# Kernel tuning notes

Measured on AMD Instinct MI355X. Metric: run time of the kernel, lower is better.

## Reference

```python
import jax, jax.numpy as jnp
import numpy as np

N, F, OUT = 8192, 256, 256


def setup_inputs() -> dict:
    key = jax.random.key(0)
    ks = jax.random.split(key, 8)
    s = 1.0 / np.sqrt(F)
    return {
        "features": jax.random.normal(ks[0], (N, F), jnp.float32),
        "key_features": jax.random.normal(ks[1], (N, F), jnp.float32),
        "adj_matrix": jax.random.uniform(ks[2], (N, N), jnp.float32),
        "W_d": jax.random.normal(ks[3], (2 * F, F), jnp.float32) * (1.0 / np.sqrt(2 * F)),
        "b_d": jnp.zeros((F,), jnp.float32),
        "W_o": jax.random.normal(ks[4], (F, OUT), jnp.float32) * s,
        "b_o": jnp.zeros((OUT,), jnp.float32),
        "W_a": jax.random.normal(ks[5], (F, F), jnp.float32) * s,
        "b_a": jnp.zeros((F,), jnp.float32),
        "W_ao": jax.random.normal(ks[6], (F, OUT), jnp.float32) * s,
        "b_ao": jnp.zeros((OUT,), jnp.float32),
    }


def reference(features, key_features, adj_matrix, W_d, b_d, W_o, b_o, W_a, b_a, W_ao, b_ao):
    n = features.shape[0]
    # masked softmax over rows; self-loop (diagonal) masked out
    neg = jnp.asarray(-1e9, adj_matrix.dtype)
    logits = adj_matrix * 5.0 + jnp.eye(n, dtype=adj_matrix.dtype) * neg
    a = jax.nn.softmax(logits, axis=-1)  # [N, N]
    # sum_j a_ij * concat(x_i, x_j) == concat(x_i * rowsum_i, (A @ X)_i)
    rowsum = jnp.sum(a, axis=-1, keepdims=True)  # == 1, kept for faithfulness
    agg = a @ features  # [N, F]
    neigh = jnp.concatenate([features * rowsum, agg], axis=-1)  # [N, 2F]
    neigh_distill = neigh @ W_d + b_d
    feature_updated = jnp.tanh((features - neigh_distill) @ W_o + b_o)
    # aggregate branch (withAgg=True)
    key_agg = (a @ key_features) @ W_a + b_a
    feature_aggregate = jnp.tanh((key_features + key_agg) @ W_ao + b_ao)
    return (feature_updated, feature_aggregate)
```

## Files before the change

### kernel.cpp

```cpp
#include <hip/hip_runtime.h>
#include <stdint.h>
#include <math.h>


typedef __attribute__((ext_vector_type(8)))  short bf16x8_t;
typedef __attribute__((ext_vector_type(4)))  float f32x4_t;
typedef __attribute__((ext_vector_type(16))) float f32x16_t;

#define MFMA32(A, B, C) __builtin_amdgcn_mfma_f32_32x32x16_bf16(A, B, C, 0, 0, 0)
#define MFMA16(A, B, C) __builtin_amdgcn_mfma_f32_16x16x32_bf16(A, B, C, 0, 0, 0)

__device__ __forceinline__ unsigned short f2bf(float x) {
    union { float f; unsigned u; } c; c.f = x;
    unsigned u = c.u;
    return (unsigned short)((u + 0x7fffu + ((u >> 16) & 1u)) >> 16);
}

__global__ __launch_bounds__(256) void transpose_f32_bf16(
    const float* __restrict__ src, unsigned short* __restrict__ dst, int R, int C)
{
    __shared__ float tile[32][33];
    const int x  = threadIdx.x & 31;
    const int y4 = (threadIdx.x >> 5) * 4;
    const int r0 = blockIdx.x * 32;
    const int c0 = blockIdx.y * 32;
#pragma unroll
    for (int i = 0; i < 4; ++i)
        tile[y4 + i][x] = src[(size_t)(r0 + y4 + i) * C + c0 + x];
    __syncthreads();
#pragma unroll
    for (int i = 0; i < 4; ++i)
        dst[(size_t)(c0 + y4 + i) * R + r0 + x] = f2bf(tile[x][y4 + i]);
}

__global__ __launch_bounds__(256) void pack_feat(
    const float* __restrict__ src, unsigned short* __restrict__ dst)
{
    const size_t idx = (size_t)blockIdx.x * 256 + threadIdx.x;
    const size_t row = idx >> 8;
    const int col = (int)(idx & 255);
    dst[row * 512 + col] = f2bf(src[idx]);
}

#define NITER 128

__device__ __forceinline__ void stage_tile(float4 v, int j2, int kbase, int skoff,
                                           int sgrow, unsigned short* sp, float& rs)
{
    float e0 = __expf(5.f * v.x);
    float e1 = __expf(5.f * v.y);
    float e2 = __expf(5.f * v.z);
    float e3 = __expf(5.f * v.w);
    const int gk = kbase + j2 * 32 + skoff;
    if (gk + 0 == sgrow) e0 = 0.f;
    if (gk + 1 == sgrow) e1 = 0.f;
    if (gk + 2 == sgrow) e2 = 0.f;
    if (gk + 3 == sgrow) e3 = 0.f;
    rs += (e0 + e1) + (e2 + e3);
    uint2 p;
    p.x = (unsigned)f2bf(e0) | ((unsigned)f2bf(e1) << 16);
    p.y = (unsigned)f2bf(e2) | ((unsigned)f2bf(e3) << 16);
    *(uint2*)sp = p;
}

__global__ __launch_bounds__(512) void exp_gemm(
    const float* __restrict__ adj, const unsigned short* __restrict__ Xt,
    float* __restrict__ Upart, float* __restrict__ sSpart)
{
    __shared__ unsigned short sA[4][64 * 32];

    const int t    = threadIdx.x;
    const int w    = t >> 6;
    const int lane = t & 63;
    const int q    = lane >> 5;
    const int l31  = lane & 31;
    const int rblk = blockIdx.x >> 1;
    const int h    = blockIdx.x & 1;
    const int row0 = rblk * 64;
    const int kbase = h * 4096;

    const int srow  = t >> 3;
    const int skoff = (t & 7) * 4;
    const int sgrow = row0 + srow;
    const float* adj_row = adj + (size_t)sgrow * 8192 + kbase + skoff;
    unsigned short* sWp = &sA[0][0] + srow * 32 + skoff;

    const unsigned short* bptr0 = Xt + (size_t)(w * 64 + l31) * 8192 + kbase + q * 8;
    const unsigned short* bptr1 = bptr0 + (size_t)32 * 8192;

    float rs = 0.f;
    f32x16_t acc[2][2];
#pragma unroll
    for (int a = 0; a < 2; ++a)
#pragma unroll
        for (int b = 0; b < 2; ++b)
#pragma unroll
            for (int e = 0; e < 16; ++e) acc[a][b][e] = 0.f;

    float4   qa[4];
    bf16x8_t bq[2][2][2];

#define LOADB(J, PAR) do {                                                  \
        int jc_ = (J); if (jc_ >= NITER) jc_ = 0;                           \
        bq[PAR][0][0] = *(const bf16x8_t*)(bptr0 + (size_t)jc_ * 32);       \
        bq[PAR][0][1] = *(const bf16x8_t*)(bptr0 + (size_t)jc_ * 32 + 16);  \
        bq[PAR][1][0] = *(const bf16x8_t*)(bptr1 + (size_t)jc_ * 32);       \
        bq[PAR][1][1] = *(const bf16x8_t*)(bptr1 + (size_t)jc_ * 32 + 16);  \
    } while (0)

    qa[0] = *(const float4*)(adj_row + 0);
    qa[1] = *(const float4*)(adj_row + 32);
    qa[2] = *(const float4*)(adj_row + 64);
    qa[3] = *(const float4*)(adj_row + 96);
    stage_tile(qa[0], 0, kbase, skoff, sgrow, sWp + 0 * 2048, rs);
    stage_tile(qa[1], 1, kbase, skoff, sgrow, sWp + 1 * 2048, rs);
    LOADB(0, 0);
    asm volatile("s_waitcnt lgkmcnt(0)\n\ts_barrier" ::: "memory");

    for (int ib = 0; ib < NITER; ib += 4) {
#pragma unroll
        for (int u = 0; u < 4; ++u) {
            const int i = ib + u;
            {
                int j = i + 4; if (j >= NITER) j = 0;
                qa[u] = *(const float4*)(adj_row + (size_t)j * 32);
            }
            LOADB(i + 1, (u + 1) & 1);
            if (i + 2 < NITER)
                stage_tile(qa[(u + 2) & 3], i + 2, kbase, skoff, sgrow,
                           sWp + ((u + 2) & 3) * 2048, rs);
            asm volatile("s_waitcnt lgkmcnt(0)\n\ts_barrier" ::: "memory");
            const unsigned short* sa = &sA[u][0];
            const int ao = l31 * 32 + q * 8;
            bf16x8_t a00 = *(const bf16x8_t*)(sa + ao);
            bf16x8_t a01 = *(const bf16x8_t*)(sa + ao + 16);
            bf16x8_t a10 = *(const bf16x8_t*)(sa + ao + 1024);
            bf16x8_t a11 = *(const bf16x8_t*)(sa + ao + 1024 + 16);
            const int p = u & 1;
            acc[0][0] = MFMA32(a00, bq[p][0][0], acc[0][0]);
            acc[1][0] = MFMA32(a10, bq[p][0][0], acc[1][0]);
            acc[0][1] = MFMA32(a00, bq[p][1][0], acc[0][1]);
            acc[1][1] = MFMA32(a10, bq[p][1][0], acc[1][1]);
            acc[0][0] = MFMA32(a01, bq[p][0][1], acc[0][0]);
            acc[1][0] = MFMA32(a11, bq[p][0][1], acc[1][0]);
            acc[0][1] = MFMA32(a01, bq[p][1][1], acc[0][1]);
            acc[1][1] = MFMA32(a11, bq[p][1][1], acc[1][1]);
        }
    }
#undef LOADB

    rs += __shfl_xor(rs, 1);
    rs += __shfl_xor(rs, 2);
    rs += __shfl_xor(rs, 4);
    if ((t & 7) == 0) sSpart[h * 8192 + row0 + (t >> 3)] = rs;

    float* up = Upart + (size_t)h * 8192 * 512 + (size_t)row0 * 512;
#pragma unroll
    for (int mt = 0; mt < 2; ++mt)
#pragma unroll
        for (int nt = 0; nt < 2; ++nt) {
            const int col = w * 64 + nt * 32 + l31;
#pragma unroll
            for (int reg = 0; reg < 16; ++reg) {
                const int lrow = (reg & 3) + 8 * (reg >> 2) + 4 * q + mt * 32;
                up[(size_t)lrow * 512 + col] = acc[mt][nt][reg];
            }
        }
}

__global__ __launch_bounds__(256) void finalize_agg(
    const float* __restrict__ Upart, const float* __restrict__ sSpart,
    unsigned short* __restrict__ XcatN, unsigned short* __restrict__ Kagg)
{
    const int row = blockIdx.x;
    const int t = threadIdx.x;
    const float* u0 = Upart + (size_t)row * 512;
    const float* u1 = u0 + (size_t)8192 * 512;
    const float inv = 1.f / (sSpart[row] + sSpart[8192 + row]);
    const float aggv  = (u0[t]       + u1[t])       * inv;
    const float kaggv = (u0[t + 256] + u1[t + 256]) * inv;
    XcatN[(size_t)row * 512 + 256 + t] = f2bf(aggv);
    Kagg [(size_t)row * 256 + t]       = f2bf(kaggv);
}

template <int EPI>
__global__ __launch_bounds__(256) void gemm_small(
    const unsigned short* __restrict__ A, const unsigned short* __restrict__ Wt,
    const float* __restrict__ bias, const float* __restrict__ aux,
    void* __restrict__ outp, int K)
{
    __shared__ unsigned short sA[32 * 32];
    __shared__ unsigned short sB[256 * 32];
    __shared__ float sBias[256];

    const int t = threadIdx.x;
    const int w = t >> 6, lane = t & 63;
    const int m_lo = lane & 15, quad = lane >> 4;
    const int row0 = blockIdx.x * 32;
    sBias[t] = bias[t];

    f32x4_t acc[2][4];
#pragma unroll
    for (int a = 0; a < 2; ++a)
#pragma unroll
        for (int b = 0; b < 4; ++b)
#pragma unroll
            for (int e = 0; e < 4; ++e) acc[a][b][e] = 0.f;

    const int nsteps = K >> 5;
    for (int ks = 0; ks < nsteps; ++ks) {
        const int k0 = ks * 32;
        __syncthreads();
        if (t < 128) {
            bf16x8_t v = *(const bf16x8_t*)(A + (size_t)(row0 + (t >> 2)) * K + k0 + (t & 3) * 8);
            *(bf16x8_t*)(&sA[(t >> 2) * 32 + (t & 3) * 8]) = v;
        }
        {
            const unsigned short* src = Wt + (size_t)t * K + k0;
            unsigned short* dst = &sB[t * 32];
            *(bf16x8_t*)(dst +  0) = *(const bf16x8_t*)(src +  0);
            *(bf16x8_t*)(dst +  8) = *(const bf16x8_t*)(src +  8);
            *(bf16x8_t*)(dst + 16) = *(const bf16x8_t*)(src + 16);
            *(bf16x8_t*)(dst + 24) = *(const bf16x8_t*)(src + 24);
        }
        __syncthreads();
        bf16x8_t a0 = *(const bf16x8_t*)(&sA[m_lo * 32 + quad * 8]);
        bf16x8_t a1 = *(const bf16x8_t*)(&sA[(16 + m_lo) * 32 + quad * 8]);
#pragma unroll
        for (int nt = 0; nt < 4; ++nt) {
            bf16x8_t b = *(const bf16x8_t*)(&sB[(w * 64 + nt * 16 + m_lo) * 32 + quad * 8]);
            acc[0][nt] = MFMA16(a0, b, acc[0][nt]);
            acc[1][nt] = MFMA16(a1, b, acc[1][nt]);
        }
    }

#pragma unroll
    for (int mt = 0; mt < 2; ++mt)
#pragma unroll
        for (int nt = 0; nt < 4; ++nt) {
            const int col = w * 64 + nt * 16 + m_lo;
#pragma unroll
            for (int r = 0; r < 4; ++r) {
                const int row = row0 + mt * 16 + quad * 4 + r;
                const float c = acc[mt][nt][r] + sBias[col];
                if (EPI == 0)
                    ((unsigned short*)outp)[(size_t)row * 256 + col] =
                        f2bf(aux[(size_t)row * 256 + col] - c);
                else if (EPI == 1)
                    ((unsigned short*)outp)[(size_t)row * 256 + col] =
                        f2bf(aux[(size_t)row * 256 + col] + c);
                else
                    ((float*)outp)[(size_t)row * 256 + col] = tanhf(c);
            }
        }
}

extern "C" void kernel_launch(void* const* d_in, const int* in_sizes, int n_in,
                              void* d_out, int out_size, void* d_ws, size_t ws_size,
                              hipStream_t stream) {
    const float* features = (const float*)d_in[0];
    const float* key      = (const float*)d_in[1];
    const float* adj      = (const float*)d_in[2];
    const float* W_d  = (const float*)d_in[3];
    const float* b_d  = (const float*)d_in[4];
    const float* W_o  = (const float*)d_in[5];
    const float* b_o  = (const float*)d_in[6];
    const float* W_a  = (const float*)d_in[7];
    const float* b_a  = (const float*)d_in[8];
    const float* W_ao = (const float*)d_in[9];
    const float* b_ao = (const float*)d_in[10];

    float* out1 = (float*)d_out;
    float* out2 = out1 + (size_t)8192 * 256;

    char* ws = (char*)d_ws;
    unsigned short* Xt    = (unsigned short*)(ws);
    unsigned short* XcatN = (unsigned short*)(ws +  8388608);
    unsigned short* Kagg  = (unsigned short*)(ws + 16777216);
    float*          Upart = (float*)        (ws + 20971520);
    float*          sSp   = (float*)        (ws + 54525952);
    unsigned short* Wd_t  = (unsigned short*)(ws + 54591488);
    unsigned short* Wo_t  = (unsigned short*)(ws + 54853632);
    unsigned short* Wa_t  = (unsigned short*)(ws + 54984704);
    unsigned short* Wao_t = (unsigned short*)(ws + 55115776);
    unsigned short* R     = Xt;
    unsigned short* Kin   = (unsigned short*)(ws + 4194304);

    dim3 blk(256);
    transpose_f32_bf16<<<dim3(256, 8), blk, 0, stream>>>(features, Xt, 8192, 256);
    transpose_f32_bf16<<<dim3(256, 8), blk, 0, stream>>>(key, Xt + (size_t)256 * 8192, 8192, 256);
    transpose_f32_bf16<<<dim3(16, 8),  blk, 0, stream>>>(W_d,  Wd_t,  512, 256);
    transpose_f32_bf16<<<dim3(8, 8),   blk, 0, stream>>>(W_o,  Wo_t,  256, 256);
    transpose_f32_bf16<<<dim3(8, 8),   blk, 0, stream>>>(W_a,  Wa_t,  256, 256);
    transpose_f32_bf16<<<dim3(8, 8),   blk, 0, stream>>>(W_ao, Wao_t, 256, 256);
    pack_feat<<<8192, blk, 0, stream>>>(features, XcatN);

    exp_gemm<<<256, dim3(512), 0, stream>>>(adj, Xt, Upart, sSp);
    finalize_agg<<<8192, blk, 0, stream>>>(Upart, sSp, XcatN, Kagg);

    gemm_small<0><<<256, blk, 0, stream>>>(XcatN, Wd_t, b_d, features, (void*)R,   512);
    gemm_small<1><<<256, blk, 0, stream>>>(Kagg,  Wa_t, b_a, key,      (void*)Kin, 256);
    gemm_small<2><<<256, blk, 0, stream>>>(R,     Wo_t, b_o, nullptr,  (void*)out1, 256);
    gemm_small<2><<<256, blk, 0, stream>>>(Kin,   Wao_t, b_ao, nullptr, (void*)out2, 256);
}
```

Baseline: 614.0 us.

## Fold linear weight chains into composed matrices and retile the exp-GEMM kernel

```diff
diff --git a/kernel.cpp b/kernel.cpp
--- a/kernel.cpp
+++ b/kernel.cpp
@@ -3,6 +3,7 @@
 #include <math.h>
 
 
+typedef __attribute__((ext_vector_type(4)))  short bf16x4_t;
 typedef __attribute__((ext_vector_type(8)))  short bf16x8_t;
 typedef __attribute__((ext_vector_type(4)))  float f32x4_t;
 typedef __attribute__((ext_vector_type(16))) float f32x16_t;
@@ -14,6 +15,15 @@
     union { float f; unsigned u; } c; c.f = x;
     unsigned u = c.u;
     return (unsigned short)((u + 0x7fffu + ((u >> 16) & 1u)) >> 16);
+}
+__device__ __forceinline__ unsigned pack2bf(float a, float b) {
+    return (unsigned)f2bf(a) | ((unsigned)f2bf(b) << 16);
+}
+__device__ __forceinline__ float bflo(unsigned u) {
+    union { unsigned u; float f; } c; c.u = u << 16; return c.f;
+}
+__device__ __forceinline__ float bfhi(unsigned u) {
+    union { unsigned u; float f; } c; c.u = u & 0xffff0000u; return c.f;
 }
 
 __global__ __launch_bounds__(256) void transpose_f32_bf16(
@@ -33,171 +43,213 @@
         dst[(size_t)(c0 + y4 + i) * R + r0 + x] = f2bf(tile[x][y4 + i]);
 }
 
-__global__ __launch_bounds__(256) void pack_feat(
-    const float* __restrict__ src, unsigned short* __restrict__ dst)
-{
-    const size_t idx = (size_t)blockIdx.x * 256 + threadIdx.x;
-    const size_t row = idx >> 8;
-    const int col = (int)(idx & 255);
-    dst[row * 512 + col] = f2bf(src[idx]);
-}
-
-#define NITER 128
-
-__device__ __forceinline__ void stage_tile(float4 v, int j2, int kbase, int skoff,
-                                           int sgrow, unsigned short* sp, float& rs)
-{
-    float e0 = __expf(5.f * v.x);
-    float e1 = __expf(5.f * v.y);
-    float e2 = __expf(5.f * v.z);
-    float e3 = __expf(5.f * v.w);
-    const int gk = kbase + j2 * 32 + skoff;
-    if (gk + 0 == sgrow) e0 = 0.f;
-    if (gk + 1 == sgrow) e1 = 0.f;
-    if (gk + 2 == sgrow) e2 = 0.f;
-    if (gk + 3 == sgrow) e3 = 0.f;
-    rs += (e0 + e1) + (e2 + e3);
-    uint2 p;
-    p.x = (unsigned)f2bf(e0) | ((unsigned)f2bf(e1) << 16);
-    p.y = (unsigned)f2bf(e2) | ((unsigned)f2bf(e3) << 16);
-    *(uint2*)sp = p;
-}
-
-__global__ __launch_bounds__(512) void exp_gemm(
+__global__ __launch_bounds__(256) void pack_half(
+    const float* __restrict__ src, unsigned* __restrict__ dst)
+{
+    const int idx = blockIdx.x * 256 + threadIdx.x;
+    const int row = idx >> 7, cp = idx & 127;
+    float2 v = *(const float2*)(src + (size_t)row * 256 + cp * 2);
+    dst[(size_t)row * 256 + cp] = pack2bf(v.x, v.y);
+}
+
+__global__ __launch_bounds__(256) void compose1(
+    const float* __restrict__ W_d, const float* __restrict__ W_o,
+    unsigned short* __restrict__ W1t)
+{
+    __shared__ float wrow[256];
+    const int k = blockIdx.x, t = threadIdx.x;
+    wrow[t] = W_d[(size_t)k * 256 + t];
+    __syncthreads();
+    float acc = 0.f;
+#pragma unroll 8
+    for (int m = 0; m < 256; ++m) acc = fmaf(wrow[m], W_o[(size_t)m * 256 + t], acc);
+    const float v = (k < 256 ? W_o[(size_t)k * 256 + t] : 0.f) - acc;
+    W1t[(size_t)t * 512 + k] = f2bf(v);
+}
+
+__global__ __launch_bounds__(256) void compose2(
+    const float* __restrict__ W_a, const float* __restrict__ W_ao,
+    unsigned short* __restrict__ W2t)
+{
+    __shared__ float wrow[256];
+    const int k = blockIdx.x, t = threadIdx.x;
+    float v;
+    if (k < 256) {
+        v = W_ao[(size_t)k * 256 + t];
+    } else {
+        wrow[t] = W_a[(size_t)(k - 256) * 256 + t];
+        __syncthreads();
+        float acc = 0.f;
+#pragma unroll 8
+        for (int m = 0; m < 256; ++m) acc = fmaf(wrow[m], W_ao[(size_t)m * 256 + t], acc);
+        v = acc;
+    }
+    W2t[(size_t)t * 512 + k] = f2bf(v);
+}
+
+__global__ __launch_bounds__(256) void biasC(
+    const float* __restrict__ b_d, const float* __restrict__ b_o,
+    const float* __restrict__ b_a, const float* __restrict__ b_ao,
+    const float* __restrict__ W_o, const float* __restrict__ W_ao,
+    float* __restrict__ c1, float* __restrict__ c2)
+{
+    const int t = threadIdx.x;
+    float a1 = 0.f, a2 = 0.f;
+#pragma unroll 8
+    for (int m = 0; m < 256; ++m) {
+        a1 = fmaf(b_d[m], W_o [(size_t)m * 256 + t], a1);
+        a2 = fmaf(b_a[m], W_ao[(size_t)m * 256 + t], a2);
+    }
+    c1[t] = b_o[t] - a1;
+    c2[t] = b_ao[t] + a2;
+}
+
+#define ROWS 128
+#define KSLICE 2048
+#define NIT 64
+#define NCH 16
+#define ASTRIDE 36
+
+__global__ __launch_bounds__(1024) void exp_gemm(
     const float* __restrict__ adj, const unsigned short* __restrict__ Xt,
-    float* __restrict__ Upart, float* __restrict__ sSpart)
-{
-    __shared__ unsigned short sA[4][64 * 32];
-
-    const int t    = threadIdx.x;
-    const int w    = t >> 6;
-    const int lane = t & 63;
-    const int q    = lane >> 5;
-    const int l31  = lane & 31;
-    const int rblk = blockIdx.x >> 1;
-    const int h    = blockIdx.x & 1;
-    const int row0 = rblk * 64;
-    const int kbase = h * 4096;
-
-    const int srow  = t >> 3;
-    const int skoff = (t & 7) * 4;
+    unsigned short* __restrict__ Upart, float* __restrict__ sSp)
+{
+    __shared__ unsigned short sA[2][4][ROWS * ASTRIDE];
+
+    const int t = threadIdx.x;
+    const int w = t >> 6, lane = t & 63, q = lane >> 5, l31 = lane & 31;
+    const int rb = blockIdx.x >> 2, h = blockIdx.x & 3;
+    const int row0 = rb * ROWS, kbase = h * KSLICE;
+
+    const int srow = t >> 3, skoff = (t & 7) * 4;
     const int sgrow = row0 + srow;
     const float* adj_row = adj + (size_t)sgrow * 8192 + kbase + skoff;
-    unsigned short* sWp = &sA[0][0] + srow * 32 + skoff;
-
-    const unsigned short* bptr0 = Xt + (size_t)(w * 64 + l31) * 8192 + kbase + q * 8;
-    const unsigned short* bptr1 = bptr0 + (size_t)32 * 8192;
+    const int swoff = srow * ASTRIDE + skoff;
+
+    const unsigned short* bptr = Xt + (size_t)(w * 32 + l31) * 8192 + kbase + q * 8;
 
     float rs = 0.f;
-    f32x16_t acc[2][2];
-#pragma unroll
-    for (int a = 0; a < 2; ++a)
-#pragma unroll
-        for (int b = 0; b < 2; ++b)
-#pragma unroll
-            for (int e = 0; e < 16; ++e) acc[a][b][e] = 0.f;
-
-    float4   qa[4];
-    bf16x8_t bq[2][2][2];
-
-#define LOADB(J, PAR) do {                                                  \
-        int jc_ = (J); if (jc_ >= NITER) jc_ = 0;                           \
-        bq[PAR][0][0] = *(const bf16x8_t*)(bptr0 + (size_t)jc_ * 32);       \
-        bq[PAR][0][1] = *(const bf16x8_t*)(bptr0 + (size_t)jc_ * 32 + 16);  \
-        bq[PAR][1][0] = *(const bf16x8_t*)(bptr1 + (size_t)jc_ * 32);       \
-        bq[PAR][1][1] = *(const bf16x8_t*)(bptr1 + (size_t)jc_ * 32 + 16);  \
-    } while (0)
-
-    qa[0] = *(const float4*)(adj_row + 0);
-    qa[1] = *(const float4*)(adj_row + 32);
-    qa[2] = *(const float4*)(adj_row + 64);
-    qa[3] = *(const float4*)(adj_row + 96);
-    stage_tile(qa[0], 0, kbase, skoff, sgrow, sWp + 0 * 2048, rs);
-    stage_tile(qa[1], 1, kbase, skoff, sgrow, sWp + 1 * 2048, rs);
-    LOADB(0, 0);
+    f32x16_t acc[4];
+#pragma unroll
+    for (int mt = 0; mt < 4; ++mt)
+#pragma unroll
+        for (int e = 0; e < 16; ++e) acc[mt][e] = 0.f;
+
+    bf16x8_t bq[4][2];
+    float4 qaA[4], qaB[4];
+
+    auto stageChunk = [&](int cidx, const float4 (&qa)[4], int buf) {
+        unsigned short* sb = &sA[buf][0][0] + swoff;
+#pragma unroll
+        for (int ks = 0; ks < 4; ++ks) {
+            const float4 v = qa[ks];
+            float e0 = __expf(5.f * v.x);
+            float e1 = __expf(5.f * v.y);
+            float e2 = __expf(5.f * v.z);
+            float e3 = __expf(5.f * v.w);
+            const int gk = kbase + (cidx * 4 + ks) * 32 + skoff;
+            if (gk + 0 == sgrow) e0 = 0.f;
+            if (gk + 1 == sgrow) e1 = 0.f;
+            if (gk + 2 == sgrow) e2 = 0.f;
+            if (gk + 3 == sgrow) e3 = 0.f;
+            rs += (e0 + e1) + (e2 + e3);
+            uint2 p; p.x = pack2bf(e0, e1); p.y = pack2bf(e2, e3);
+            *(uint2*)(sb + ks * (ROWS * ASTRIDE)) = p;
+        }
+    };
+
+    auto phase = [&](int c, float4 (&qaPre)[4], const float4 (&qaStg)[4], int buf) {
+        if (c + 2 < NCH) {
+#pragma unroll
+            for (int ks = 0; ks < 4; ++ks)
+                qaPre[ks] = *(const float4*)(adj_row + (size_t)((c + 2) * 4 + ks) * 32);
+        }
+        if (c + 1 < NCH) stageChunk(c + 1, qaStg, buf ^ 1);
+#pragma unroll
+        for (int u = 0; u < 4; ++u) {
+            const int j = c * 4 + u;
+            int jn = j + 2; if (jn >= NIT) jn = 0;
+            bq[(u + 2) & 3][0] = *(const bf16x8_t*)(bptr + (size_t)jn * 32);
+            bq[(u + 2) & 3][1] = *(const bf16x8_t*)(bptr + (size_t)jn * 32 + 16);
+            const unsigned short* sa = &sA[buf][u][0] + l31 * ASTRIDE + q * 8;
+#pragma unroll
+            for (int s = 0; s < 2; ++s)
+#pragma unroll
+                for (int mt = 0; mt < 4; ++mt) {
+                    const unsigned short* p = sa + mt * (32 * ASTRIDE) + s * 16;
+                    bf16x4_t lo = *(const bf16x4_t*)p;
+                    bf16x4_t hi = *(const bf16x4_t*)(p + 4);
+                    bf16x8_t a = __builtin_shufflevector(lo, hi, 0, 1, 2, 3, 4, 5, 6, 7);
+                    acc[mt] = MFMA32(a, bq[u][s], acc[mt]);
+                }
+        }
+        asm volatile("s_waitcnt lgkmcnt(0)\n\ts_barrier" ::: "memory");
+    };
+
+#pragma unroll
+    for (int ks = 0; ks < 4; ++ks)
+        qaA[ks] = *(const float4*)(adj_row + (size_t)ks * 32);
+#pragma unroll
+    for (int ks = 0; ks < 4; ++ks)
+        qaB[ks] = *(const float4*)(adj_row + (size_t)(4 + ks) * 32);
+    stageChunk(0, qaA, 0);
+    bq[0][0] = *(const bf16x8_t*)(bptr + 0);
+    bq[0][1] = *(const bf16x8_t*)(bptr + 16);
+    bq[1][0] = *(const bf16x8_t*)(bptr + 32);
+    bq[1][1] = *(const bf16x8_t*)(bptr + 48);
     asm volatile("s_waitcnt lgkmcnt(0)\n\ts_barrier" ::: "memory");
 
-    for (int ib = 0; ib < NITER; ib += 4) {
-#pragma unroll
-        for (int u = 0; u < 4; ++u) {
-            const int i = ib + u;
-            {
-                int j = i + 4; if (j >= NITER) j = 0;
-                qa[u] = *(const float4*)(adj_row + (size_t)j * 32);
-            }
-            LOADB(i + 1, (u + 1) & 1);
-            if (i + 2 < NITER)
-                stage_tile(qa[(u + 2) & 3], i + 2, kbase, skoff, sgrow,
-                           sWp + ((u + 2) & 3) * 2048, rs);
-            asm volatile("s_waitcnt lgkmcnt(0)\n\ts_barrier" ::: "memory");
-            const unsigned short* sa = &sA[u][0];
-            const int ao = l31 * 32 + q * 8;
-            bf16x8_t a00 = *(const bf16x8_t*)(sa + ao);
-            bf16x8_t a01 = *(const bf16x8_t*)(sa + ao + 16);
-            bf16x8_t a10 = *(const bf16x8_t*)(sa + ao + 1024);
-            bf16x8_t a11 = *(const bf16x8_t*)(sa + ao + 1024 + 16);
-            const int p = u & 1;
-            acc[0][0] = MFMA32(a00, bq[p][0][0], acc[0][0]);
-            acc[1][0] = MFMA32(a10, bq[p][0][0], acc[1][0]);
-            acc[0][1] = MFMA32(a00, bq[p][1][0], acc[0][1]);
-            acc[1][1] = MFMA32(a10, bq[p][1][0], acc[1][1]);
-            acc[0][0] = MFMA32(a01, bq[p][0][1], acc[0][0]);
-            acc[1][0] = MFMA32(a11, bq[p][0][1], acc[1][0]);
-            acc[0][1] = MFMA32(a01, bq[p][1][1], acc[0][1]);
-            acc[1][1] = MFMA32(a11, bq[p][1][1], acc[1][1]);
-        }
-    }
-#undef LOADB
+    for (int c0 = 0; c0 < NCH; c0 += 2) {
+        phase(c0,     qaA, qaB, 0);
+        phase(c0 + 1, qaB, qaA, 1);
+    }
 
     rs += __shfl_xor(rs, 1);
     rs += __shfl_xor(rs, 2);
     rs += __shfl_xor(rs, 4);
-    if ((t & 7) == 0) sSpart[h * 8192 + row0 + (t >> 3)] = rs;
-
-    float* up = Upart + (size_t)h * 8192 * 512 + (size_t)row0 * 512;
-#pragma unroll
-    for (int mt = 0; mt < 2; ++mt)
-#pragma unroll
-        for (int nt = 0; nt < 2; ++nt) {
-            const int col = w * 64 + nt * 32 + l31;
-#pragma unroll
-            for (int reg = 0; reg < 16; ++reg) {
-                const int lrow = (reg & 3) + 8 * (reg >> 2) + 4 * q + mt * 32;
-                up[(size_t)lrow * 512 + col] = acc[mt][nt][reg];
-            }
+    if ((t & 7) == 0) sSp[h * 8192 + sgrow] = rs;
+
+    unsigned short* up = Upart + (size_t)h * (8192 * 512) + (size_t)row0 * 512 + (w * 32 + l31);
+#pragma unroll
+    for (int mt = 0; mt < 4; ++mt)
+#pragma unroll
+        for (int reg = 0; reg < 16; ++reg) {
+            const int lrow = mt * 32 + (reg & 3) + 8 * (reg >> 2) + 4 * q;
+            up[(size_t)lrow * 512] = f2bf(acc[mt][reg]);
         }
 }
 
 __global__ __launch_bounds__(256) void finalize_agg(
-    const float* __restrict__ Upart, const float* __restrict__ sSpart,
-    unsigned short* __restrict__ XcatN, unsigned short* __restrict__ Kagg)
-{
-    const int row = blockIdx.x;
-    const int t = threadIdx.x;
-    const float* u0 = Upart + (size_t)row * 512;
-    const float* u1 = u0 + (size_t)8192 * 512;
-    const float inv = 1.f / (sSpart[row] + sSpart[8192 + row]);
-    const float aggv  = (u0[t]       + u1[t])       * inv;
-    const float kaggv = (u0[t + 256] + u1[t + 256]) * inv;
-    XcatN[(size_t)row * 512 + 256 + t] = f2bf(aggv);
-    Kagg [(size_t)row * 256 + t]       = f2bf(kaggv);
-}
-
-template <int EPI>
-__global__ __launch_bounds__(256) void gemm_small(
+    const unsigned* __restrict__ Upart, const float* __restrict__ sSp,
+    unsigned* __restrict__ XcatN, unsigned* __restrict__ Kcat)
+{
+    const int row = blockIdx.x, t = threadIdx.x;
+    const float inv = 1.f / (sSp[row] + sSp[8192 + row] + sSp[16384 + row] + sSp[24576 + row]);
+    const unsigned* u = Upart + (size_t)row * 256 + t;
+    float lo = 0.f, hi = 0.f;
+#pragma unroll
+    for (int hh = 0; hh < 4; ++hh) {
+        const unsigned v = u[(size_t)hh * (8192 * 256)];
+        lo += bflo(v); hi += bfhi(v);
+    }
+    const unsigned res = pack2bf(lo * inv, hi * inv);
+    if (t < 128) XcatN[(size_t)row * 256 + 128 + t] = res;
+    else         Kcat [(size_t)row * 256 + t];
+    if (t >= 128) Kcat[(size_t)row * 256 + t] = res;
+}
+
+__global__ __launch_bounds__(256) void gemm_out(
     const unsigned short* __restrict__ A, const unsigned short* __restrict__ Wt,
-    const float* __restrict__ bias, const float* __restrict__ aux,
-    void* __restrict__ outp, int K)
-{
-    __shared__ unsigned short sA[32 * 32];
-    __shared__ unsigned short sB[256 * 32];
+    const float* __restrict__ cvec, float* __restrict__ out)
+{
+    __shared__ unsigned short sAm[32 * ASTRIDE];
+    __shared__ unsigned short sB[256 * ASTRIDE];
     __shared__ float sBias[256];
 
-    const int t = threadIdx.x;
-    const int w = t >> 6, lane = t & 63;
+    const int t = threadIdx.x, w = t >> 6, lane = t & 63;
     const int m_lo = lane & 15, quad = lane >> 4;
     const int row0 = blockIdx.x * 32;
-    sBias[t] = bias[t];
+    sBias[t] = cvec[t];
 
     f32x4_t acc[2][4];
 #pragma unroll
@@ -207,28 +259,40 @@
 #pragma unroll
             for (int e = 0; e < 4; ++e) acc[a][b][e] = 0.f;
 
-    const int nsteps = K >> 5;
-    for (int ks = 0; ks < nsteps; ++ks) {
+    for (int ks = 0; ks < 16; ++ks) {
         const int k0 = ks * 32;
         __syncthreads();
         if (t < 128) {
-            bf16x8_t v = *(const bf16x8_t*)(A + (size_t)(row0 + (t >> 2)) * K + k0 + (t & 3) * 8);
-            *(bf16x8_t*)(&sA[(t >> 2) * 32 + (t & 3) * 8]) = v;
+            bf16x8_t v = *(const bf16x8_t*)(A + (size_t)(row0 + (t >> 2)) * 512 + k0 + (t & 3) * 8);
+            unsigned short* d = &sAm[(t >> 2) * ASTRIDE + (t & 3) * 8];
+            *(bf16x4_t*)d       = __builtin_shufflevector(v, v, 0, 1, 2, 3);
+            *(bf16x4_t*)(d + 4) = __builtin_shufflevector(v, v, 4, 5, 6, 7);
         }
         {
-            const unsigned short* src = Wt + (size_t)t * K + k0;
-            unsigned short* dst = &sB[t * 32];
-            *(bf16x8_t*)(dst +  0) = *(const bf16x8_t*)(src +  0);
-            *(bf16x8_t*)(dst +  8) = *(const bf16x8_t*)(src +  8);
-            *(bf16x8_t*)(dst + 16) = *(const bf16x8_t*)(src + 16);
-            *(bf16x8_t*)(dst + 24) = *(const bf16x8_t*)(src + 24);
+            const unsigned short* src = Wt + (size_t)t * 512 + k0;
+            unsigned short* d = &sB[t * ASTRIDE];
+#pragma unroll
+            for (int j = 0; j < 4; ++j) {
+                bf16x8_t v = *(const bf16x8_t*)(src + j * 8);
+                *(bf16x4_t*)(d + j * 8)     = __builtin_shufflevector(v, v, 0, 1, 2, 3);
+                *(bf16x4_t*)(d + j * 8 + 4) = __builtin_shufflevector(v, v, 4, 5, 6, 7);
+            }
         }
         __syncthreads();
-        bf16x8_t a0 = *(const bf16x8_t*)(&sA[m_lo * 32 + quad * 8]);
-        bf16x8_t a1 = *(const bf16x8_t*)(&sA[(16 + m_lo) * 32 + quad * 8]);
+        bf16x8_t a0, a1;
+        {
+            const unsigned short* p = &sAm[m_lo * ASTRIDE + quad * 8];
+            bf16x4_t lo = *(const bf16x4_t*)p, hi = *(const bf16x4_t*)(p + 4);
+            a0 = __builtin_shufflevector(lo, hi, 0, 1, 2, 3, 4, 5, 6, 7);
+            p += 16 * ASTRIDE;
+            lo = *(const bf16x4_t*)p; hi = *(const bf16x4_t*)(p + 4);
+            a1 = __builtin_shufflevector(lo, hi, 0, 1, 2, 3, 4, 5, 6, 7);
+        }
 #pragma unroll
         for (int nt = 0; nt < 4; ++nt) {
-            bf16x8_t b = *(const bf16x8_t*)(&sB[(w * 64 + nt * 16 + m_lo) * 32 + quad * 8]);
+            const unsigned short* p = &sB[(w * 64 + nt * 16 + m_lo) * ASTRIDE + quad * 8];
+            bf16x4_t lo = *(const bf16x4_t*)p, hi = *(const bf16x4_t*)(p + 4);
+            bf16x8_t b = __builtin_shufflevector(lo, hi, 0, 1, 2, 3, 4, 5, 6, 7);
             acc[0][nt] = MFMA16(a0, b, acc[0][nt]);
             acc[1][nt] = MFMA16(a1, b, acc[1][nt]);
         }
@@ -242,15 +306,7 @@
 #pragma unroll
             for (int r = 0; r < 4; ++r) {
                 const int row = row0 + mt * 16 + quad * 4 + r;
-                const float c = acc[mt][nt][r] + sBias[col];
-                if (EPI == 0)
-                    ((unsigned short*)outp)[(size_t)row * 256 + col] =
-                        f2bf(aux[(size_t)row * 256 + col] - c);
-                else if (EPI == 1)
-                    ((unsigned short*)outp)[(size_t)row * 256 + col] =
-                        f2bf(aux[(size_t)row * 256 + col] + c);
-                else
-                    ((float*)outp)[(size_t)row * 256 + col] = tanhf(c);
+                out[(size_t)row * 256 + col] = tanhf(acc[mt][nt][r] + sBias[col]);
             }
         }
 }
@@ -274,32 +330,29 @@
     float* out2 = out1 + (size_t)8192 * 256;
 
     char* ws = (char*)d_ws;
-    unsigned short* Xt    = (unsigned short*)(ws);
-    unsigned short* XcatN = (unsigned short*)(ws +  8388608);
-    unsigned short* Kagg  = (unsigned short*)(ws + 16777216);
-    float*          Upart = (float*)        (ws + 20971520);
-    float*          sSp   = (float*)        (ws + 54525952);
-    unsigned short* Wd_t  = (unsigned short*)(ws + 54591488);
-    unsigned short* Wo_t  = (unsigned short*)(ws + 54853632);
-    unsigned short* Wa_t  = (unsigned short*)(ws + 54984704);
-    unsigned short* Wao_t = (unsigned short*)(ws + 55115776);
-    unsigned short* R     = Xt;
-    unsigned short* Kin   = (unsigned short*)(ws + 4194304);
+    unsigned short* XcatN = (unsigned short*)(ws);
+    unsigned short* Kcat  = (unsigned short*)(ws +  8388608);
+    unsigned short* Xt    = (unsigned short*)(ws + 16777216);
+    unsigned short* Upart = (unsigned short*)(ws + 25165824);
+    float*          sSp   = (float*)         (ws + 58720256);
+    unsigned short* W1t   = (unsigned short*)(ws + 58851328);
+    unsigned short* W2t   = (unsigned short*)(ws + 59113472);
+    float*          c1    = (float*)         (ws + 59375616);
+    float*          c2    = (float*)         (ws + 59376640);
 
     dim3 blk(256);
     transpose_f32_bf16<<<dim3(256, 8), blk, 0, stream>>>(features, Xt, 8192, 256);
     transpose_f32_bf16<<<dim3(256, 8), blk, 0, stream>>>(key, Xt + (size_t)256 * 8192, 8192, 256);
-    transpose_f32_bf16<<<dim3(16, 8),  blk, 0, stream>>>(W_d,  Wd_t,  512, 256);
-    transpose_f32_bf16<<<dim3(8, 8),   blk, 0, stream>>>(W_o,  Wo_t,  256, 256);
-    transpose_f32_bf16<<<dim3(8, 8),   blk, 0, stream>>>(W_a,  Wa_t,  256, 256);
-    transpose_f32_bf16<<<dim3(8, 8),   blk, 0, stream>>>(W_ao, Wao_t, 256, 256);
-    pack_feat<<<8192, blk, 0, stream>>>(features, XcatN);
-
-    exp_gemm<<<256, dim3(512), 0, stream>>>(adj, Xt, Upart, sSp);
-    finalize_agg<<<8192, blk, 0, stream>>>(Upart, sSp, XcatN, Kagg);
-
-    gemm_small<0><<<256, blk, 0, stream>>>(XcatN, Wd_t, b_d, features, (void*)R,   512);
-    gemm_small<1><<<256, blk, 0, stream>>>(Kagg,  Wa_t, b_a, key,      (void*)Kin, 256);
-    gemm_small<2><<<256, blk, 0, stream>>>(R,     Wo_t, b_o, nullptr,  (void*)out1, 256);
-    gemm_small<2><<<256, blk, 0, stream>>>(Kin,   Wao_t, b_ao, nullptr, (void*)out2, 256);
-}
+    pack_half<<<4096, blk, 0, stream>>>(features, (unsigned*)XcatN);
+    pack_half<<<4096, blk, 0, stream>>>(key, (unsigned*)Kcat);
+    compose1<<<512, blk, 0, stream>>>(W_d, W_o, W1t);
+    compose2<<<512, blk, 0, stream>>>(W_a, W_ao, W2t);
+    biasC<<<1, blk, 0, stream>>>(b_d, b_o, b_a, b_ao, W_o, W_ao, c1, c2);
+
+    exp_gemm<<<256, dim3(1024), 0, stream>>>(adj, Xt, Upart, sSp);
+    finalize_agg<<<8192, blk, 0, stream>>>((const unsigned*)Upart, sSp,
+                                           (unsigned*)XcatN, (unsigned*)Kcat);
+
+    gemm_out<<<256, blk, 0, stream>>>(XcatN, W1t, c1, out1);
+    gemm_out<<<256, blk, 0, stream>>>(Kcat,  W2t, c2, out2);
+}
```

New measurement: 590.3 us. -3.9%, faster.
